# Performance work log

Measured on AMD Instinct MI355X. Metric: run time of the kernel, lower is better.

## Reference

```python
import jax, jax.numpy as jnp
import numpy as np

B, N, H, W = 64, 32, 200, 200


def setup_inputs() -> dict:
    key = jax.random.key(0)
    k1, k2, k3, k4 = jax.random.split(key, 4)
    return {
        "parameter": jax.random.uniform(k1, (B, N, 3), dtype=jnp.float32),
        "x_start": jax.random.uniform(k2, (), dtype=jnp.float32),
        "y_start": jax.random.uniform(k3, (), dtype=jnp.float32),
        "theta": jax.random.uniform(k4, (), dtype=jnp.float32, minval=-3.14159, maxval=3.14159),
        # learned parameters at their torch init values
        "weights": jnp.eye(2, dtype=jnp.float32),
        "biases": jnp.zeros(2, dtype=jnp.float32),
        "thick_mult": jnp.array(0.5, dtype=jnp.float32),
        "thick_bias": jnp.array(0.1, dtype=jnp.float32),
        "dark_exp": jnp.array(1.0, dtype=jnp.float32),
        "dark_non_lin_weight": jnp.array(0.5, dtype=jnp.float32),
        "x_m": jnp.array(1.0, dtype=jnp.float32),
        "y_m": jnp.array(1.0, dtype=jnp.float32),
        "x_b": jnp.array(0.0, dtype=jnp.float32),
        "y_b": jnp.array(0.0, dtype=jnp.float32),
        "use_conv": 0,
    }


def reference(parameter, x_start, y_start, theta, weights, biases, thick_mult,
              thick_bias, dark_exp, dark_non_lin_weight, x_m, y_m, x_b, y_b,
              use_conv):
    # torch.flip(traj, dims=(2,)) then traj[:,:,0] *= -1:
    # channel0 (y) = -parameter[...,1], channel1 (x) = parameter[...,0]
    y0 = -parameter[..., 1]
    x0 = parameter[..., 0]
    # rotation about origin (vectorized over batch; identical per-element math)
    c, s = jnp.cos(theta), jnp.sin(theta)
    x_rot = x0 * c + y0 * s
    y_rot = -x0 * s + y0 * c
    yy = y_rot * y_m + y_b + y_start
    xx = x_rot * x_m + x_b + x_start
    traj = jnp.stack([yy, xx], axis=-1)                      # (B,N,2)
    # curve_to_stroke: matmul(weights, curve).T + biases == traj @ weights.T + biases
    strokes = traj @ weights.T + biases                      # (B,N,2)
    thick = (parameter[..., 2] * 2.0 + 0.5) / 64.0           # (B,N)
    # grid_coords: channel0 = row/H, channel1 = col/W
    gy = jnp.arange(H, dtype=strokes.dtype) / H
    gx = jnp.arange(W, dtype=strokes.dtype) / W
    coords = jnp.stack(jnp.meshgrid(gy, gx, indexing='ij'), axis=-1)  # (H,W,2)
    v = strokes[:, :-1, None, None, :]                       # (B,N-1,1,1,2)
    w = strokes[:, 1:, None, None, :]
    p = coords[None, None]                                   # (1,1,H,W,2)
    wv = w - v
    d2 = jnp.sum(wv * wv, axis=-1)                           # (B,N-1,1,1)
    dot = jnp.sum((p - v) * wv, axis=-1) / (d2 + 1e-5)       # (B,N-1,H,W)
    frac = jnp.clip(dot, 0.0, 1.0)
    proj = v + frac[..., None] * wv                          # (B,N-1,H,W,2)
    diff = p - proj
    dist = jnp.sqrt(jnp.sum(diff * diff, axis=-1))           # (B,N-1,H,W)
    th = thick[:, :-1, None, None] * (1.0 - frac) + thick[:, 1:, None, None] * frac
    th = jnp.maximum(th * thick_mult + thick_bias, 1e-8)
    dark = jnp.clip((th - dist) / th, 0.0, 1.0)
    dark = (dark + 1e-4) ** dark_exp
    nl = jax.nn.sigmoid(dark * 16.0 - 8.0)
    dark = dark_non_lin_weight * nl + (1.0 - dark_non_lin_weight) * dark
    return jnp.max(dark, axis=1)                             # (B,H,W)
```

## Files before the change

kernel.cpp:

```cpp
#include <hip/hip_runtime.h>
#include <math.h>

#define B_ 64
#define N_ 32
#define H_ 200
#define W_ 200
#define NSEG (N_ - 1)
#define TSX 32
#define TSY 16
#define NTX 7
#define NTY 13
#define TILE_RAD 0.087f

__global__ __launch_bounds__(256) void stroke_kernel(
    const float* __restrict__ param,
    const float* __restrict__ x_start,
    const float* __restrict__ y_start,
    const float* __restrict__ theta,
    const float* __restrict__ weights,
    const float* __restrict__ biases,
    const float* __restrict__ thick_mult,
    const float* __restrict__ thick_bias,
    const float* __restrict__ dark_exp_p,
    const float* __restrict__ dark_nlw_p,
    const float* __restrict__ x_m_p,
    const float* __restrict__ y_m_p,
    const float* __restrict__ x_b_p,
    const float* __restrict__ y_b_p,
    float* __restrict__ out)
{
    __shared__ float4 s_A[NSEG];
    __shared__ float4 s_B[NSEG];
    __shared__ int s_cnt;

    const int b   = blockIdx.z;
    const int tid = threadIdx.x;

    const float dexp = dark_exp_p[0], dnlw = dark_nlw_p[0];

    if (tid < 64) {
        float sy = 0.0f, sx = 0.0f, tk = 0.0f;
        const float tm = thick_mult[0], tb = thick_bias[0];
        if (tid < N_) {
            const float thv = theta[0];
            const float c   = cosf(thv), s = sinf(thv);
            const float xs  = x_start[0], ys = y_start[0];
            const float W00 = weights[0], W01 = weights[1];
            const float W10 = weights[2], W11 = weights[3];
            const float bb0 = biases[0],  bb1 = biases[1];
            const float xm  = x_m_p[0], ym = y_m_p[0];
            const float xb  = x_b_p[0], yb = y_b_p[0];
            float p0 = param[(b * N_ + tid) * 3 + 0];
            float p1 = param[(b * N_ + tid) * 3 + 1];
            float p2 = param[(b * N_ + tid) * 3 + 2];
            float x0 = p0, y0 = -p1;
            float x_rot =  x0 * c + y0 * s;
            float y_rot = -x0 * s + y0 * c;
            float yy = y_rot * ym + yb + ys;
            float xx = x_rot * xm + xb + xs;
            sy = yy * W00 + xx * W01 + bb0;
            sx = yy * W10 + xx * W11 + bb1;
            tk = (p2 * 2.0f + 0.5f) * (1.0f / 64.0f);
        }
        float sy1 = __shfl_down(sy, 1);
        float sx1 = __shfl_down(sx, 1);
        float tk1 = __shfl_down(tk, 1);

        bool keep = false;
        float4 A4 = make_float4(0,0,0,0), B4 = make_float4(0,0,0,0);
        if (tid < NSEG) {
            float wvy = sy1 - sy, wvx = sx1 - sx;
            float d2 = wvy * wvy + wvx * wvx;
            float inv_d2 = 1.0f / (d2 + 1e-5f);
            float c0 = tk * tm + tb;
            float c1 = (tk1 - tk) * tm;
            A4 = make_float4(sy, sx, wvy, wvx);
            B4 = make_float4(inv_d2, c0, c1, wvx * inv_d2 * (1.0f / W_));
            const float cy = ((float)(blockIdx.y * TSY) + 7.5f)  * (1.0f / H_);
            const float cx = ((float)(blockIdx.x * TSX) + 15.5f) * (1.0f / W_);
            float dyc = cy - sy, dxc = cx - sx;
            float dot = (dyc * wvy + dxc * wvx) * inv_d2;
            float fr  = fminf(fmaxf(dot, 0.0f), 1.0f);
            float ey  = dyc - fr * wvy;
            float ex  = dxc - fr * wvx;
            float e2c = ey * ey + ex * ex;
            float thmax = fmaxf(fmaxf(c0, c0 + c1), 1e-8f);
            float reach = thmax + TILE_RAD;
            keep = e2c < reach * reach;
        }
        unsigned long long mask = __ballot(keep);
        int pos = (int)__popcll(mask & ((1ull << tid) - 1ull));
        if (keep) { s_A[pos] = A4; s_B[pos] = B4; }
        if (tid == 0) s_cnt = (int)__popcll(mask);
    }
    __syncthreads();

    const int cnt = s_cnt;
    const int ii = tid >> 4, jj = tid & 15;
    const int i  = blockIdx.y * TSY + ii;
    const int j0 = blockIdx.x * TSX + (jj << 1);
    const float py  = (float)i  * (1.0f / H_);
    const float px0 = (float)j0 * (1.0f / W_);
    const float px1 = px0 + (1.0f / W_);

    const bool hoist = (dexp > 0.0f) && (dnlw >= 0.0f) && (dnlw <= 1.0f);

    float r0, r1;
    if (hoist) {
        float q0m = INFINITY, q1m = INFINITY;
        if (cnt > 0) {
            float4 A = s_A[0], Bc = s_B[0];
            for (int n = 0; n < cnt; ++n) {
                int np = (n + 1 < cnt) ? n + 1 : n;
                float4 An = s_A[np], Bn = s_B[np];
                float dy  = py  - A.x;
                float dx0 = px0 - A.y;
                float dx1 = px1 - A.y;
                float dot0 = fmaf(dy, A.z, dx0 * A.w) * Bc.x;
                float dot1 = dot0 + Bc.w;
                float fr0 = __builtin_amdgcn_fmed3f(dot0, 0.0f, 1.0f);
                float fr1 = __builtin_amdgcn_fmed3f(dot1, 0.0f, 1.0f);
                float ey0 = fmaf(-fr0, A.z, dy);
                float ex0 = fmaf(-fr0, A.w, dx0);
                float e20 = fmaf(ey0, ey0, ex0 * ex0);
                float th0 = fmaxf(fmaf(fr0, Bc.z, Bc.y), 1e-8f);
                float it0 = __builtin_amdgcn_rcpf(th0);
                q0m = fminf(q0m, (e20 * it0) * it0);
                float ey1 = fmaf(-fr1, A.z, dy);
                float ex1 = fmaf(-fr1, A.w, dx1);
                float e21 = fmaf(ey1, ey1, ex1 * ex1);
                float th1 = fmaxf(fmaf(fr1, Bc.z, Bc.y), 1e-8f);
                float it1 = __builtin_amdgcn_rcpf(th1);
                q1m = fminf(q1m, (e21 * it1) * it1);
                A = An; Bc = Bn;
            }
        }
        {
            float md = fminf(fmaxf(1.0f - __builtin_amdgcn_sqrtf(q0m), 0.0f), 1.0f);
            float d  = __expf(dexp * __logf(md + 1e-4f));
            float nl = __builtin_amdgcn_rcpf(1.0f + __expf(8.0f - d * 16.0f));
            r0 = dnlw * nl + (1.0f - dnlw) * d;
        }
        {
            float md = fminf(fmaxf(1.0f - __builtin_amdgcn_sqrtf(q1m), 0.0f), 1.0f);
            float d  = __expf(dexp * __logf(md + 1e-4f));
            float nl = __builtin_amdgcn_rcpf(1.0f + __expf(8.0f - d * 16.0f));
            r1 = dnlw * nl + (1.0f - dnlw) * d;
        }
    } else {
        float b0 = -INFINITY, b1 = -INFINITY;
        if (cnt < NSEG) {
            float d0  = __expf(dexp * __logf(1e-4f));
            float nl0 = __builtin_amdgcn_rcpf(1.0f + __expf(8.0f - d0 * 16.0f));
            float t0  = dnlw * nl0 + (1.0f - dnlw) * d0;
            b0 = t0; b1 = t0;
        }
        for (int n = 0; n < cnt; ++n) {
            float4 A = s_A[n], Bc = s_B[n];
            float dy  = py  - A.x;
            float dx0 = px0 - A.y;
            float dx1 = px1 - A.y;
            float dot0 = fmaf(dy, A.z, dx0 * A.w) * Bc.x;
            float dot1 = dot0 + Bc.w;
            float fr0 = __builtin_amdgcn_fmed3f(dot0, 0.0f, 1.0f);
            float fr1 = __builtin_amdgcn_fmed3f(dot1, 0.0f, 1.0f);
            {
                float ey = fmaf(-fr0, A.z, dy);
                float ex = fmaf(-fr0, A.w, dx0);
                float dist = __builtin_amdgcn_sqrtf(fmaf(ey, ey, ex * ex));
                float th = fmaxf(fmaf(fr0, Bc.z, Bc.y), 1e-8f);
                float dark = fminf(fmaxf(fmaf(-dist, __builtin_amdgcn_rcpf(th), 1.0f), 0.0f), 1.0f);
                float d  = __expf(dexp * __logf(dark + 1e-4f));
                float nl = __builtin_amdgcn_rcpf(1.0f + __expf(8.0f - d * 16.0f));
                b0 = fmaxf(b0, dnlw * nl + (1.0f - dnlw) * d);
            }
            {
                float ey = fmaf(-fr1, A.z, dy);
                float ex = fmaf(-fr1, A.w, dx1);
                float dist = __builtin_amdgcn_sqrtf(fmaf(ey, ey, ex * ex));
                float th = fmaxf(fmaf(fr1, Bc.z, Bc.y), 1e-8f);
                float dark = fminf(fmaxf(fmaf(-dist, __builtin_amdgcn_rcpf(th), 1.0f), 0.0f), 1.0f);
                float d  = __expf(dexp * __logf(dark + 1e-4f));
                float nl = __builtin_amdgcn_rcpf(1.0f + __expf(8.0f - d * 16.0f));
                b1 = fmaxf(b1, dnlw * nl + (1.0f - dnlw) * d);
            }
        }
        r0 = b0; r1 = b1;
    }

    if (i < H_ && j0 < W_) {
        *reinterpret_cast<float2*>(&out[(b * H_ + i) * W_ + j0]) = make_float2(r0, r1);
    }
}

extern "C" void kernel_launch(void* const* d_in, const int* in_sizes, int n_in,
                              void* d_out, int out_size, void* d_ws, size_t ws_size,
                              hipStream_t stream) {
    const float* param      = (const float*)d_in[0];
    const float* x_start    = (const float*)d_in[1];
    const float* y_start    = (const float*)d_in[2];
    const float* theta      = (const float*)d_in[3];
    const float* weights    = (const float*)d_in[4];
    const float* biases     = (const float*)d_in[5];
    const float* thick_mult = (const float*)d_in[6];
    const float* thick_bias = (const float*)d_in[7];
    const float* dark_exp   = (const float*)d_in[8];
    const float* dark_nlw   = (const float*)d_in[9];
    const float* x_m        = (const float*)d_in[10];
    const float* y_m        = (const float*)d_in[11];
    const float* x_b        = (const float*)d_in[12];
    const float* y_b        = (const float*)d_in[13];
    float* out = (float*)d_out;

    dim3 block(256);
    dim3 grid(NTX, NTY, B_);
    stroke_kernel<<<grid, block, 0, stream>>>(
        param, x_start, y_start, theta, weights, biases,
        thick_mult, thick_bias, dark_exp, dark_nlw,
        x_m, y_m, x_b, y_b, out);
}
```

Before: 14.37 us.

## Enlarge tiles to 32x32 with four pixels per thread and drop block barrier

Each block now covers a 32x32 tile, and each thread computes four pixels (two columns by two rows 16 apart). The second row's projection dot is derived incrementally from the first, so segment setup work is shared across more pixels. Every wave now redundantly computes segment culling and writes identical data to shared memory. This replaces the single-wave setup plus __syncthreads with a local lgkmcnt wait. The epilogue skips exp/log when dark_exp equals 1. The cost is a larger tile culling radius, so more segments survive per tile, and setup work is duplicated across waves.

```diff
diff --git a/kernel.cpp b/kernel.cpp
--- a/kernel.cpp
+++ b/kernel.cpp
@@ -6,11 +6,9 @@
 #define H_ 200
 #define W_ 200
 #define NSEG (N_ - 1)
-#define TSX 32
-#define TSY 16
-#define NTX 7
-#define NTY 13
-#define TILE_RAD 0.087f
+#define TS 32
+#define NT 7
+#define TILE_RAD 0.111f
 
 __global__ __launch_bounds__(256) void stroke_kernel(
     const float* __restrict__ param,
@@ -31,165 +29,161 @@
 {
     __shared__ float4 s_A[NSEG];
     __shared__ float4 s_B[NSEG];
-    __shared__ int s_cnt;
-
-    const int b   = blockIdx.z;
-    const int tid = threadIdx.x;
+
+    const int b    = blockIdx.z;
+    const int tid  = threadIdx.x;
+    const int lane = tid & 63;
 
     const float dexp = dark_exp_p[0], dnlw = dark_nlw_p[0];
 
-    if (tid < 64) {
-        float sy = 0.0f, sx = 0.0f, tk = 0.0f;
-        const float tm = thick_mult[0], tb = thick_bias[0];
-        if (tid < N_) {
-            const float thv = theta[0];
-            const float c   = cosf(thv), s = sinf(thv);
-            const float xs  = x_start[0], ys = y_start[0];
-            const float W00 = weights[0], W01 = weights[1];
-            const float W10 = weights[2], W11 = weights[3];
-            const float bb0 = biases[0],  bb1 = biases[1];
-            const float xm  = x_m_p[0], ym = y_m_p[0];
-            const float xb  = x_b_p[0], yb = y_b_p[0];
-            float p0 = param[(b * N_ + tid) * 3 + 0];
-            float p1 = param[(b * N_ + tid) * 3 + 1];
-            float p2 = param[(b * N_ + tid) * 3 + 2];
-            float x0 = p0, y0 = -p1;
-            float x_rot =  x0 * c + y0 * s;
-            float y_rot = -x0 * s + y0 * c;
-            float yy = y_rot * ym + yb + ys;
-            float xx = x_rot * xm + xb + xs;
-            sy = yy * W00 + xx * W01 + bb0;
-            sx = yy * W10 + xx * W11 + bb1;
-            tk = (p2 * 2.0f + 0.5f) * (1.0f / 64.0f);
-        }
-        float sy1 = __shfl_down(sy, 1);
-        float sx1 = __shfl_down(sx, 1);
-        float tk1 = __shfl_down(tk, 1);
-
-        bool keep = false;
-        float4 A4 = make_float4(0,0,0,0), B4 = make_float4(0,0,0,0);
-        if (tid < NSEG) {
-            float wvy = sy1 - sy, wvx = sx1 - sx;
-            float d2 = wvy * wvy + wvx * wvx;
-            float inv_d2 = 1.0f / (d2 + 1e-5f);
-            float c0 = tk * tm + tb;
-            float c1 = (tk1 - tk) * tm;
-            A4 = make_float4(sy, sx, wvy, wvx);
-            B4 = make_float4(inv_d2, c0, c1, wvx * inv_d2 * (1.0f / W_));
-            const float cy = ((float)(blockIdx.y * TSY) + 7.5f)  * (1.0f / H_);
-            const float cx = ((float)(blockIdx.x * TSX) + 15.5f) * (1.0f / W_);
-            float dyc = cy - sy, dxc = cx - sx;
-            float dot = (dyc * wvy + dxc * wvx) * inv_d2;
-            float fr  = fminf(fmaxf(dot, 0.0f), 1.0f);
-            float ey  = dyc - fr * wvy;
-            float ex  = dxc - fr * wvx;
-            float e2c = ey * ey + ex * ex;
-            float thmax = fmaxf(fmaxf(c0, c0 + c1), 1e-8f);
-            float reach = thmax + TILE_RAD;
-            keep = e2c < reach * reach;
-        }
-        unsigned long long mask = __ballot(keep);
-        int pos = (int)__popcll(mask & ((1ull << tid) - 1ull));
-        if (keep) { s_A[pos] = A4; s_B[pos] = B4; }
-        if (tid == 0) s_cnt = (int)__popcll(mask);
-    }
-    __syncthreads();
-
-    const int cnt = s_cnt;
+    float sy = 0.0f, sx = 0.0f, tk = 0.0f;
+    const float tm = thick_mult[0], tb = thick_bias[0];
+    if (lane < N_) {
+        const float thv = theta[0];
+        const float c   = __cosf(thv), s = __sinf(thv);
+        const float xs  = x_start[0], ys = y_start[0];
+        const float W00 = weights[0], W01 = weights[1];
+        const float W10 = weights[2], W11 = weights[3];
+        const float bb0 = biases[0],  bb1 = biases[1];
+        const float xm  = x_m_p[0], ym = y_m_p[0];
+        const float xb  = x_b_p[0], yb = y_b_p[0];
+        float p0 = param[(b * N_ + lane) * 3 + 0];
+        float p1 = param[(b * N_ + lane) * 3 + 1];
+        float p2 = param[(b * N_ + lane) * 3 + 2];
+        float x0 = p0, y0 = -p1;
+        float x_rot =  x0 * c + y0 * s;
+        float y_rot = -x0 * s + y0 * c;
+        float yy = y_rot * ym + yb + ys;
+        float xx = x_rot * xm + xb + xs;
+        sy = yy * W00 + xx * W01 + bb0;
+        sx = yy * W10 + xx * W11 + bb1;
+        tk = (p2 * 2.0f + 0.5f) * (1.0f / 64.0f);
+    }
+    float sy1 = __shfl_down(sy, 1);
+    float sx1 = __shfl_down(sx, 1);
+    float tk1 = __shfl_down(tk, 1);
+
+    bool keep = false;
+    float4 A4 = make_float4(0,0,0,0), B4 = make_float4(0,0,0,0);
+    if (lane < NSEG) {
+        float wvy = sy1 - sy, wvx = sx1 - sx;
+        float d2 = wvy * wvy + wvx * wvx;
+        float inv_d2 = 1.0f / (d2 + 1e-5f);
+        float c0 = tk * tm + tb;
+        float c1 = (tk1 - tk) * tm;
+        A4 = make_float4(sy, sx, wvy, wvx);
+        B4 = make_float4(inv_d2, c0, c1, wvx * inv_d2 * (1.0f / W_));
+        const float cy = ((float)(blockIdx.y * TS) + 15.5f) * (1.0f / H_);
+        const float cx = ((float)(blockIdx.x * TS) + 15.5f) * (1.0f / W_);
+        float dyc = cy - sy, dxc = cx - sx;
+        float dot = (dyc * wvy + dxc * wvx) * inv_d2;
+        float fr  = __builtin_amdgcn_fmed3f(dot, 0.0f, 1.0f);
+        float ey  = dyc - fr * wvy;
+        float ex  = dxc - fr * wvx;
+        float e2c = ey * ey + ex * ex;
+        float thmax = fmaxf(fmaxf(c0, c0 + c1), 1e-8f);
+        float reach = thmax + TILE_RAD;
+        keep = e2c < reach * reach;
+    }
+    unsigned long long mask = __ballot(keep);
+    const int cnt = (int)__popcll(mask);
+    if (keep) {
+        int pos = (int)__popcll(mask & ((1ull << lane) - 1ull));
+        s_A[pos] = A4; s_B[pos] = B4;
+    }
+    asm volatile("s_waitcnt lgkmcnt(0)" ::: "memory");
+
     const int ii = tid >> 4, jj = tid & 15;
-    const int i  = blockIdx.y * TSY + ii;
-    const int j0 = blockIdx.x * TSX + (jj << 1);
-    const float py  = (float)i  * (1.0f / H_);
-    const float px0 = (float)j0 * (1.0f / W_);
-    const float px1 = px0 + (1.0f / W_);
+    const int r0 = blockIdx.y * TS + ii;
+    const int c0 = blockIdx.x * TS + (jj << 1);
+    const float py0 = (float)r0 * (1.0f / H_);
+    const float py1 = py0 + 16.0f / H_;
+    const float px0 = (float)c0 * (1.0f / W_);
+    const float px1 = px0 + 1.0f / W_;
 
     const bool hoist = (dexp > 0.0f) && (dnlw >= 0.0f) && (dnlw <= 1.0f);
 
-    float r0, r1;
+    float r00, r01, r10, r11;
     if (hoist) {
-        float q0m = INFINITY, q1m = INFINITY;
+        float q00 = INFINITY, q01 = INFINITY, q10 = INFINITY, q11 = INFINITY;
         if (cnt > 0) {
             float4 A = s_A[0], Bc = s_B[0];
             for (int n = 0; n < cnt; ++n) {
                 int np = (n + 1 < cnt) ? n + 1 : n;
                 float4 An = s_A[np], Bn = s_B[np];
-                float dy  = py  - A.x;
-                float dx0 = px0 - A.y;
-                float dx1 = px1 - A.y;
-                float dot0 = fmaf(dy, A.z, dx0 * A.w) * Bc.x;
-                float dot1 = dot0 + Bc.w;
-                float fr0 = __builtin_amdgcn_fmed3f(dot0, 0.0f, 1.0f);
-                float fr1 = __builtin_amdgcn_fmed3f(dot1, 0.0f, 1.0f);
-                float ey0 = fmaf(-fr0, A.z, dy);
-                float ex0 = fmaf(-fr0, A.w, dx0);
-                float e20 = fmaf(ey0, ey0, ex0 * ex0);
-                float th0 = fmaxf(fmaf(fr0, Bc.z, Bc.y), 1e-8f);
-                float it0 = __builtin_amdgcn_rcpf(th0);
-                q0m = fminf(q0m, (e20 * it0) * it0);
-                float ey1 = fmaf(-fr1, A.z, dy);
-                float ex1 = fmaf(-fr1, A.w, dx1);
-                float e21 = fmaf(ey1, ey1, ex1 * ex1);
-                float th1 = fmaxf(fmaf(fr1, Bc.z, Bc.y), 1e-8f);
-                float it1 = __builtin_amdgcn_rcpf(th1);
-                q1m = fminf(q1m, (e21 * it1) * it1);
+                float dy0 = py0 - A.x, dy1 = py1 - A.x;
+                float dx0 = px0 - A.y, dx1 = px1 - A.y;
+                float dot00 = fmaf(dy0, A.z, dx0 * A.w) * Bc.x;
+                float ddy   = (A.z * Bc.x) * (16.0f / H_);
+                float dot01 = dot00 + Bc.w;
+                float dot10 = dot00 + ddy;
+                float dot11 = dot10 + Bc.w;
+                #define PX(dotv, dyv, dxv, qm) { \
+                    float fr = __builtin_amdgcn_fmed3f(dotv, 0.0f, 1.0f); \
+                    float ey = fmaf(-fr, A.z, dyv); \
+                    float ex = fmaf(-fr, A.w, dxv); \
+                    float e2 = fmaf(ey, ey, ex * ex); \
+                    float th = fmaxf(fmaf(fr, Bc.z, Bc.y), 1e-8f); \
+                    float it = __builtin_amdgcn_rcpf(th); \
+                    qm = fminf(qm, (e2 * it) * it); }
+                PX(dot00, dy0, dx0, q00)
+                PX(dot01, dy0, dx1, q01)
+                PX(dot10, dy1, dx0, q10)
+                PX(dot11, dy1, dx1, q11)
+                #undef PX
                 A = An; Bc = Bn;
             }
         }
-        {
-            float md = fminf(fmaxf(1.0f - __builtin_amdgcn_sqrtf(q0m), 0.0f), 1.0f);
-            float d  = __expf(dexp * __logf(md + 1e-4f));
-            float nl = __builtin_amdgcn_rcpf(1.0f + __expf(8.0f - d * 16.0f));
-            r0 = dnlw * nl + (1.0f - dnlw) * d;
-        }
-        {
-            float md = fminf(fmaxf(1.0f - __builtin_amdgcn_sqrtf(q1m), 0.0f), 1.0f);
-            float d  = __expf(dexp * __logf(md + 1e-4f));
-            float nl = __builtin_amdgcn_rcpf(1.0f + __expf(8.0f - d * 16.0f));
-            r1 = dnlw * nl + (1.0f - dnlw) * d;
-        }
+        const bool lin = (dexp == 1.0f);
+        #define EPI(qm, rr) { \
+            float md = fminf(fmaxf(1.0f - __builtin_amdgcn_sqrtf(qm), 0.0f), 1.0f); \
+            float d  = lin ? (md + 1e-4f) : __expf(dexp * __logf(md + 1e-4f)); \
+            float nl = __builtin_amdgcn_rcpf(1.0f + __expf(8.0f - d * 16.0f)); \
+            rr = dnlw * nl + (1.0f - dnlw) * d; }
+        EPI(q00, r00) EPI(q01, r01) EPI(q10, r10) EPI(q11, r11)
+        #undef EPI
     } else {
-        float b0 = -INFINITY, b1 = -INFINITY;
+        float b00 = -INFINITY, b01 = -INFINITY, b10 = -INFINITY, b11 = -INFINITY;
         if (cnt < NSEG) {
             float d0  = __expf(dexp * __logf(1e-4f));
             float nl0 = __builtin_amdgcn_rcpf(1.0f + __expf(8.0f - d0 * 16.0f));
             float t0  = dnlw * nl0 + (1.0f - dnlw) * d0;
-            b0 = t0; b1 = t0;
+            b00 = b01 = b10 = b11 = t0;
         }
         for (int n = 0; n < cnt; ++n) {
             float4 A = s_A[n], Bc = s_B[n];
-            float dy  = py  - A.x;
-            float dx0 = px0 - A.y;
-            float dx1 = px1 - A.y;
-            float dot0 = fmaf(dy, A.z, dx0 * A.w) * Bc.x;
-            float dot1 = dot0 + Bc.w;
-            float fr0 = __builtin_amdgcn_fmed3f(dot0, 0.0f, 1.0f);
-            float fr1 = __builtin_amdgcn_fmed3f(dot1, 0.0f, 1.0f);
-            {
-                float ey = fmaf(-fr0, A.z, dy);
-                float ex = fmaf(-fr0, A.w, dx0);
-                float dist = __builtin_amdgcn_sqrtf(fmaf(ey, ey, ex * ex));
-                float th = fmaxf(fmaf(fr0, Bc.z, Bc.y), 1e-8f);
-                float dark = fminf(fmaxf(fmaf(-dist, __builtin_amdgcn_rcpf(th), 1.0f), 0.0f), 1.0f);
-                float d  = __expf(dexp * __logf(dark + 1e-4f));
-                float nl = __builtin_amdgcn_rcpf(1.0f + __expf(8.0f - d * 16.0f));
-                b0 = fmaxf(b0, dnlw * nl + (1.0f - dnlw) * d);
-            }
-            {
-                float ey = fmaf(-fr1, A.z, dy);
-                float ex = fmaf(-fr1, A.w, dx1);
-                float dist = __builtin_amdgcn_sqrtf(fmaf(ey, ey, ex * ex));
-                float th = fmaxf(fmaf(fr1, Bc.z, Bc.y), 1e-8f);
-                float dark = fminf(fmaxf(fmaf(-dist, __builtin_amdgcn_rcpf(th), 1.0f), 0.0f), 1.0f);
-                float d  = __expf(dexp * __logf(dark + 1e-4f));
-                float nl = __builtin_amdgcn_rcpf(1.0f + __expf(8.0f - d * 16.0f));
-                b1 = fmaxf(b1, dnlw * nl + (1.0f - dnlw) * d);
-            }
+            float dy0 = py0 - A.x, dy1 = py1 - A.x;
+            float dx0 = px0 - A.y, dx1 = px1 - A.y;
+            float dot00 = fmaf(dy0, A.z, dx0 * A.w) * Bc.x;
+            float ddy   = (A.z * Bc.x) * (16.0f / H_);
+            float dot01 = dot00 + Bc.w;
+            float dot10 = dot00 + ddy;
+            float dot11 = dot10 + Bc.w;
+            #define PXF(dotv, dyv, dxv, bb) { \
+                float fr = __builtin_amdgcn_fmed3f(dotv, 0.0f, 1.0f); \
+                float ey = fmaf(-fr, A.z, dyv); \
+                float ex = fmaf(-fr, A.w, dxv); \
+                float dist = __builtin_amdgcn_sqrtf(fmaf(ey, ey, ex * ex)); \
+                float th = fmaxf(fmaf(fr, Bc.z, Bc.y), 1e-8f); \
+                float dark = fminf(fmaxf(fmaf(-dist, __builtin_amdgcn_rcpf(th), 1.0f), 0.0f), 1.0f); \
+                float d  = __expf(dexp * __logf(dark + 1e-4f)); \
+                float nl = __builtin_amdgcn_rcpf(1.0f + __expf(8.0f - d * 16.0f)); \
+                bb = fmaxf(bb, dnlw * nl + (1.0f - dnlw) * d); }
+            PXF(dot00, dy0, dx0, b00)
+            PXF(dot01, dy0, dx1, b01)
+            PXF(dot10, dy1, dx0, b10)
+            PXF(dot11, dy1, dx1, b11)
+            #undef PXF
         }
-        r0 = b0; r1 = b1;
-    }
-
-    if (i < H_ && j0 < W_) {
-        *reinterpret_cast<float2*>(&out[(b * H_ + i) * W_ + j0]) = make_float2(r0, r1);
+        r00 = b00; r01 = b01; r10 = b10; r11 = b11;
+    }
+
+    if (c0 < W_) {
+        if (r0 < H_)
+            *reinterpret_cast<float2*>(&out[(b * H_ + r0) * W_ + c0]) = make_float2(r00, r01);
+        int r1 = r0 + 16;
+        if (r1 < H_)
+            *reinterpret_cast<float2*>(&out[(b * H_ + r1) * W_ + c0]) = make_float2(r10, r11);
     }
 }
 
@@ -213,7 +207,7 @@
     float* out = (float*)d_out;
 
     dim3 block(256);
-    dim3 grid(NTX, NTY, B_);
+    dim3 grid(NT, NT, B_);
     stroke_kernel<<<grid, block, 0, stream>>>(
         param, x_start, y_start, theta, weights, biases,
         thick_mult, thick_bias, dark_exp, dark_nlw,
```

Result: slower. 15.59 us (+8.5%).
